# Optimization experiments

Measured on AMD Instinct MI355X. Metric: run time of the kernel, lower is better.

The kernel has to match this reference:

```python
import jax, jax.numpy as jnp
import numpy as np

D_MODEL = 1024
NUM_HEADS = 16
D_K = D_MODEL // NUM_HEADS
B, S = 2, 2048


def setup_inputs() -> dict:
    key = jax.random.key(0)
    ks = jax.random.split(key, 9)
    scale = 1.0 / np.sqrt(D_MODEL)
    return {
        "hidden_states": jax.random.normal(ks[0], (B, S, D_MODEL), dtype=jnp.float32),
        "attention_mask": jnp.ones((B, S, S), dtype=jnp.int32),
        "Wq": jax.random.normal(ks[1], (D_MODEL, D_MODEL), dtype=jnp.float32) * scale,
        "bq": jnp.zeros((D_MODEL,), dtype=jnp.float32),
        "Wk": jax.random.normal(ks[2], (D_MODEL, D_MODEL), dtype=jnp.float32) * scale,
        "bk": jnp.zeros((D_MODEL,), dtype=jnp.float32),
        "Wv": jax.random.normal(ks[3], (D_MODEL, D_MODEL), dtype=jnp.float32) * scale,
        "bv": jnp.zeros((D_MODEL,), dtype=jnp.float32),
        "Wo": jax.random.normal(ks[4], (D_MODEL, D_MODEL), dtype=jnp.float32) * scale,
        "bo": jnp.zeros((D_MODEL,), dtype=jnp.float32),
    }


def reference(hidden_states, attention_mask, Wq, bq, Wk, bk, Wv, bv, Wo, bo):
    b, s, _ = hidden_states.shape
    # torch Linear: y = x @ W.T + b
    def proj(W, bias):
        y = jnp.einsum('bsd,ed->bse', hidden_states, W) + bias
        return y.reshape(b, s, NUM_HEADS, D_K).transpose(0, 2, 1, 3)  # [B,H,S,dk]
    q = proj(Wq, bq)
    k = proj(Wk, bk)
    v = proj(Wv, bv)
    scores = jnp.einsum('bnqd,bnkd->bnqk', q, k) / np.sqrt(D_K)
    mask = attention_mask[:, None, :, :]  # [B,1,S,S]
    scores = jnp.where(mask == 0, jnp.float32(-1e9), scores)
    attn = jax.nn.softmax(scores, axis=-1)  # dropout = identity (eval)
    ctx = jnp.einsum('bnqk,bnkd->bnqd', attn, v)
    ctx = ctx.transpose(0, 2, 1, 3).reshape(b, s, D_MODEL)
    return jnp.einsum('bsd,ed->bse', ctx, Wo) + bo
```

## Files before the change

### kernel.cpp

```cpp
#include <hip/hip_runtime.h>

typedef short short8 __attribute__((ext_vector_type(8)));
typedef float floatx4 __attribute__((ext_vector_type(4)));
typedef float floatx16 __attribute__((ext_vector_type(16)));
typedef unsigned short ushort4v __attribute__((ext_vector_type(4)));

#define DEV static __device__ __forceinline__

DEV unsigned short f2bf(float f) {
  unsigned int u = __builtin_bit_cast(unsigned int, f);
  u += 0x7fffu + ((u >> 16) & 1u);
  return (unsigned short)(u >> 16);
}

DEV unsigned int cvtpk(float a, float b) {
  unsigned int r;
  asm("v_cvt_pk_bf16_f32 %0, %1, %2" : "=v"(r) : "v"(a), "v"(b));
  return r;
}

DEV void gload16(const unsigned short* g, unsigned short* l) {
  __builtin_amdgcn_global_load_lds((__attribute__((address_space(1))) void*)g,
                                   (__attribute__((address_space(3))) void*)l,
                                   16, 0, 0);
}

__global__ void convert_kernel(const float* __restrict__ hs, const float* __restrict__ Wq,
                               const float* __restrict__ Wk, const float* __restrict__ Wv,
                               const float* __restrict__ Wo,
                               unsigned short* __restrict__ xbf, unsigned short* __restrict__ wqkv,
                               unsigned short* __restrict__ wobf) {
  size_t i4 = ((size_t)blockIdx.x * 256 + threadIdx.x) * 4;
  const float* src;
  unsigned short* dst;
  if (i4 < 4194304) {
    src = hs + i4; dst = xbf + i4;
  } else if (i4 < 7340032) {
    size_t o = i4 - 4194304;
    size_t lo = o & 1048575;
    src = (o < 1048576) ? (Wq + lo) : ((o < 2097152) ? (Wk + lo) : (Wv + lo));
    dst = wqkv + o;
  } else {
    size_t o = i4 - 7340032;
    src = Wo + o; dst = wobf + o;
  }
  float4 v = *(const float4*)src;
  ushort4v u;
  u.x = f2bf(v.x); u.y = f2bf(v.y); u.z = f2bf(v.z); u.w = f2bf(v.w);
  *(ushort4v*)dst = u;
}

__global__ void maskpack_kernel(const int* __restrict__ mask, unsigned long long* __restrict__ bits) {
  int w = blockIdx.x * 256 + threadIdx.x;
  const int4* p = (const int4*)(mask + (size_t)w * 64);
  unsigned long long r = 0ull;
#pragma unroll
  for (int j = 0; j < 16; ++j) {
    int4 m = p[j];
    r |= (unsigned long long)(m.x != 0) << (j * 4 + 0);
    r |= (unsigned long long)(m.y != 0) << (j * 4 + 1);
    r |= (unsigned long long)(m.z != 0) << (j * 4 + 2);
    r |= (unsigned long long)(m.w != 0) << (j * 4 + 3);
  }
  bits[w] = r;
}

__global__ void __launch_bounds__(256) qkv_gemm(
    const unsigned short* __restrict__ X, const unsigned short* __restrict__ W,
    const float* __restrict__ bq, const float* __restrict__ bk, const float* __restrict__ bv,
    unsigned short* __restrict__ Qb, unsigned short* __restrict__ Kb,
    unsigned short* __restrict__ Vt) {
  __shared__ __align__(16) unsigned short As[128 * 32];
  __shared__ __align__(16) unsigned short Bs[128 * 32];
  const int tid = threadIdx.x;
  const int lane = tid & 63, wv = tid >> 6;
  const int wm = wv >> 1, wn = wv & 1;
  const int quad = lane >> 4, l15 = lane & 15;
  const int mb = blockIdx.y, nb = blockIdx.x;
  const bool sw = (nb < 16);

  const unsigned short* ga = X + (size_t)(mb * 128 + (tid >> 2)) * 1024 + (tid & 3) * 8;
  const unsigned short* gb = W + (size_t)(nb * 128 + (tid >> 2)) * 1024 + (tid & 3) * 8;
  unsigned short* la1 = As + tid * 8;
  unsigned short* la2 = As + 2048 + tid * 8;
  unsigned short* lb1 = Bs + tid * 8;
  unsigned short* lb2 = Bs + 2048 + tid * 8;

  const int wx = sw ? wn : wm;
  const int ww = sw ? wm : wn;

  floatx4 acc[4][4] = {};
  for (int kt = 0; kt < 32; ++kt) {
    const int k0 = kt * 32;
    gload16(ga + k0, la1);
    gload16(ga + k0 + 65536, la2);
    gload16(gb + k0, lb1);
    gload16(gb + k0 + 65536, lb2);
    __syncthreads();
    short8 xa[4], wb[4];
#pragma unroll
    for (int i = 0; i < 4; ++i) {
      xa[i] = *(const short8*)&As[(wx * 64 + i * 16 + l15) * 32 + quad * 8];
      wb[i] = *(const short8*)&Bs[(ww * 64 + i * 16 + l15) * 32 + quad * 8];
    }
    if (sw) {
#pragma unroll
      for (int mt = 0; mt < 4; ++mt)
#pragma unroll
        for (int nt = 0; nt < 4; ++nt)
          acc[mt][nt] = __builtin_amdgcn_mfma_f32_16x16x32_bf16(wb[mt], xa[nt], acc[mt][nt], 0, 0, 0);
    } else {
#pragma unroll
      for (int mt = 0; mt < 4; ++mt)
#pragma unroll
        for (int nt = 0; nt < 4; ++nt)
          acc[mt][nt] = __builtin_amdgcn_mfma_f32_16x16x32_bf16(xa[mt], wb[nt], acc[mt][nt], 0, 0, 0);
    }
    __syncthreads();
  }

  if (sw) {
#pragma unroll
    for (int mt = 0; mt < 4; ++mt) {
      const int wc0 = nb * 128 + wm * 64 + mt * 16 + quad * 4;
      const int mat = wc0 >> 10;
      const int nl0 = wc0 & 1023;
      const int hh = nl0 >> 6, d0 = nl0 & 63;
      const float4 b4 = *(const float4*)((mat ? bk : bq) + nl0);
      unsigned short* dst = mat ? Kb : Qb;
#pragma unroll
      for (int nt = 0; nt < 4; ++nt) {
        const int colx = mb * 128 + wn * 64 + nt * 16 + l15;
        const int bb = colx >> 11, s = colx & 2047;
        ushort4v pv;
        pv[0] = f2bf(acc[mt][nt][0] + b4.x);
        pv[1] = f2bf(acc[mt][nt][1] + b4.y);
        pv[2] = f2bf(acc[mt][nt][2] + b4.z);
        pv[3] = f2bf(acc[mt][nt][3] + b4.w);
        *(ushort4v*)&dst[((size_t)(bb * 16 + hh) * 2048 + s) * 64 + d0] = pv;
      }
    }
  } else {
#pragma unroll
    for (int nt = 0; nt < 4; ++nt) {
      const int col = nb * 128 + wn * 64 + nt * 16 + l15;
      const int nl = col & 1023;
      const float bias = bv[nl];
      const int hh = nl >> 6, d = nl & 63;
#pragma unroll
      for (int mt = 0; mt < 4; ++mt) {
        const int row0 = mb * 128 + wm * 64 + mt * 16 + quad * 4;
        const int bb = row0 >> 11, s = row0 & 2047;
        ushort4v pv;
#pragma unroll
        for (int r = 0; r < 4; ++r) pv[r] = f2bf(acc[mt][nt][r] + bias);
        *(ushort4v*)&Vt[((size_t)(bb * 16 + hh) * 64 + d) * 2048 + s] = pv;
      }
    }
  }
}

__global__ void __launch_bounds__(256, 2) attn_kernel(
    const unsigned short* __restrict__ Qb, const unsigned short* __restrict__ Kb,
    const unsigned short* __restrict__ Vt, const unsigned long long* __restrict__ mbits,
    unsigned short* __restrict__ ctx) {
  __shared__ __align__(16) unsigned short SM[16384];
  const int tid = threadIdx.x;
  const int lane = tid & 63, wv = tid >> 6;
  const int l31 = lane & 31, h = lane >> 5;
  const int qg = wv & 1, h2 = wv >> 1;
  const int bid = (blockIdx.x & 7) * 128 + (blockIdx.x >> 3);
  const int pair = bid >> 5, qt = bid & 31;
  const int b_ = pair >> 4, hd = pair & 15;
  const int qrow = qt * 64 + qg * 32 + l31;
  const size_t pbase = (size_t)pair * (2048 * 64);
  const size_t vtb = (size_t)pair * (64 * 2048);

  short8 qf[4];
#pragma unroll
  for (int ks = 0; ks < 4; ++ks)
    qf[ks] = *(const short8*)(Qb + pbase + (size_t)qrow * 64 + ks * 16 + h * 8);

  const int kSrc = (lane >> 3) * 64 + (((lane & 7) ^ (lane >> 3)) * 8);
  const int vSrc = (lane >> 2) * 2048 + (((lane & 3) ^ ((lane >> 3) & 3)) * 8);

  const unsigned short* kgb = Kb + pbase + (size_t)h2 * (1024 * 64);
  const unsigned short* vgb = Vt + vtb + h2 * 1024;
  unsigned short* ldK = SM + h2 * 4096 + lane * 8;
  unsigned short* ldV = SM + h2 * 4096 + 2048 + lane * 8;

  const unsigned long long* mrow = mbits + ((size_t)b_ * 2048 + qrow) * 32 + h2 * 16;

  floatx16 acc_o[2] = {};
  float lsum = 0.f;
  const float SCL = 0.125f * 1.44269504088896340736f;
  const float NC = -10.0f;

  if (qg == 0) {
#pragma unroll
    for (int i = 0; i < 4; ++i) gload16(kgb + kSrc + i * 512, ldK + i * 512);
  } else {
#pragma unroll
    for (int i = 0; i < 4; ++i) gload16(vgb + vSrc + (size_t)i * 32768, ldV + i * 512);
  }
  __syncthreads();

  for (int it = 0; it < 32; ++it) {
    const int cur = it & 1;
    const unsigned short* Kh = SM + cur * 8192 + h2 * 4096;
    const unsigned short* Vh = Kh + 2048;

    if (it < 31) {
      const int nb = cur ^ 1;
      if (qg == 0) {
        const unsigned short* s = kgb + (size_t)(it + 1) * 2048 + kSrc;
        unsigned short* d = ldK + nb * 8192;
#pragma unroll
        for (int i = 0; i < 4; ++i) gload16(s + i * 512, d + i * 512);
      } else {
        const unsigned short* s = vgb + (size_t)(it + 1) * 32 + vSrc;
        unsigned short* d = ldV + nb * 8192;
#pragma unroll
        for (int i = 0; i < 4; ++i) gload16(s + (size_t)i * 32768, d + i * 512);
      }
    }
    const unsigned long long w = mrow[it >> 1];
    const int bitbase = (it & 1) * 32;

    floatx16 accs = {};
    __builtin_amdgcn_s_setprio(1);
#pragma unroll
    for (int ks = 0; ks < 4; ++ks) {
      short8 kf = *(const short8*)&Kh[l31 * 64 + (((ks * 2 + h) ^ (l31 & 7)) * 8)];
      accs = __builtin_amdgcn_mfma_f32_32x32x16_bf16(kf, qf[ks], accs, 0, 0, 0);
    }
    __builtin_amdgcn_s_setprio(0);

    if (__any(w != ~0ull)) {
#pragma unroll
      for (int reg = 0; reg < 16; ++reg) {
        const int kl = (reg & 3) + 8 * (reg >> 2) + 4 * h;
        if (!((w >> (bitbase + kl)) & 1ull)) accs[reg] = -6e9f;
      }
    }

    unsigned int pk[8];
    float ls = 0.f;
#pragma unroll
    for (int i = 0; i < 8; ++i) {
      const float a = exp2f(fmaf(accs[2 * i], SCL, NC));
      const float b = exp2f(fmaf(accs[2 * i + 1], SCL, NC));
      ls += a + b;
      pk[i] = cvtpk(a, b);
    }
    lsum += ls;
#pragma unroll
    for (int u = 0; u < 2; ++u) {
      auto r02 = __builtin_amdgcn_permlane32_swap(pk[4 * u + 0], pk[4 * u + 2], false, false);
      auto r13 = __builtin_amdgcn_permlane32_swap(pk[4 * u + 1], pk[4 * u + 3], false, false);
      union { unsigned int wd[4]; short8 s8; } af;
      af.wd[0] = r02[0];
      af.wd[1] = r13[0];
      af.wd[2] = r02[1];
      af.wd[3] = r13[1];
      __builtin_amdgcn_s_setprio(1);
#pragma unroll
      for (int nt = 0; nt < 2; ++nt) {
        const int vrow = nt * 32 + l31;
        short8 vf = *(const short8*)&Vh[vrow * 32 + (((u * 2 + h) ^ ((vrow >> 1) & 3)) * 8)];
        acc_o[nt] = __builtin_amdgcn_mfma_f32_32x32x16_bf16(af.s8, vf, acc_o[nt], 0, 0, 0);
      }
      __builtin_amdgcn_s_setprio(0);
    }
    __syncthreads();
  }

  lsum += __shfl_xor(lsum, 32);

  float* red = (float*)SM;
  if (h2 == 1) {
    float* p = red + (qg * 64 + lane) * 33;
#pragma unroll
    for (int reg = 0; reg < 16; ++reg) {
      p[reg] = acc_o[0][reg];
      p[16 + reg] = acc_o[1][reg];
    }
    p[32] = lsum;
  }
  __syncthreads();
  if (h2 == 0) {
    const float* p = red + (qg * 64 + lane) * 33;
#pragma unroll
    for (int reg = 0; reg < 16; ++reg) {
      acc_o[0][reg] += p[reg];
      acc_o[1][reg] += p[16 + reg];
    }
    lsum += p[32];
    const float rinv = 1.f / ((lsum > 0.f) ? lsum : 1.f);
#pragma unroll
    for (int reg = 0; reg < 16; ++reg) {
      const int ql = (reg & 3) + 8 * (reg >> 2) + 4 * h;
      const float rl = __shfl(rinv, ql);
      const size_t base = ((size_t)b_ * 2048 + qt * 64 + qg * 32 + ql) * 1024 + hd * 64;
      ctx[base + l31]      = f2bf(acc_o[0][reg] * rl);
      ctx[base + 32 + l31] = f2bf(acc_o[1][reg] * rl);
    }
  }
}

__global__ void __launch_bounds__(256) out_gemm(
    const unsigned short* __restrict__ C, const unsigned short* __restrict__ W,
    const float* __restrict__ bo, float* __restrict__ out) {
  __shared__ __align__(16) unsigned short As[128 * 32];
  __shared__ __align__(16) unsigned short Bs[128 * 32];
  const int tid = threadIdx.x;
  const int lane = tid & 63, wv = tid >> 6;
  const int wm = wv >> 1, wn = wv & 1;
  const int quad = lane >> 4, l15 = lane & 15;
  const int mb = blockIdx.y, nb = blockIdx.x;

  const unsigned short* ga = C + (size_t)(mb * 128 + (tid >> 2)) * 1024 + (tid & 3) * 8;
  const unsigned short* gb = W + (size_t)(nb * 128 + (tid >> 2)) * 1024 + (tid & 3) * 8;
  unsigned short* la1 = As + tid * 8;
  unsigned short* la2 = As + 2048 + tid * 8;
  unsigned short* lb1 = Bs + tid * 8;
  unsigned short* lb2 = Bs + 2048 + tid * 8;

  floatx4 acc[4][4] = {};
  for (int kt = 0; kt < 32; ++kt) {
    const int k0 = kt * 32;
    gload16(ga + k0, la1);
    gload16(ga + k0 + 65536, la2);
    gload16(gb + k0, lb1);
    gload16(gb + k0 + 65536, lb2);
    __syncthreads();
    short8 af[4], bfr[4];
#pragma unroll
    for (int i = 0; i < 4; ++i) {
      af[i]  = *(const short8*)&As[(wm * 64 + i * 16 + l15) * 32 + quad * 8];
      bfr[i] = *(const short8*)&Bs[(wn * 64 + i * 16 + l15) * 32 + quad * 8];
    }
#pragma unroll
    for (int mt = 0; mt < 4; ++mt)
#pragma unroll
      for (int nt = 0; nt < 4; ++nt)
        acc[mt][nt] = __builtin_amdgcn_mfma_f32_16x16x32_bf16(af[mt], bfr[nt], acc[mt][nt], 0, 0, 0);
    __syncthreads();
  }
#pragma unroll
  for (int nt = 0; nt < 4; ++nt) {
    const int col = nb * 128 + wn * 64 + nt * 16 + l15;
    const float bias = bo[col];
#pragma unroll
    for (int mt = 0; mt < 4; ++mt)
#pragma unroll
      for (int r = 0; r < 4; ++r) {
        const int row = mb * 128 + wm * 64 + mt * 16 + quad * 4 + r;
        out[(size_t)row * 1024 + col] = acc[mt][nt][r] + bias;
      }
  }
}

extern "C" void kernel_launch(void* const* d_in, const int* in_sizes, int n_in,
                              void* d_out, int out_size, void* d_ws, size_t ws_size,
                              hipStream_t stream) {
  const float* hs = (const float*)d_in[0];
  const int* mask = (const int*)d_in[1];
  const float* Wq = (const float*)d_in[2];
  const float* bq = (const float*)d_in[3];
  const float* Wk = (const float*)d_in[4];
  const float* bk = (const float*)d_in[5];
  const float* Wv = (const float*)d_in[6];
  const float* bv = (const float*)d_in[7];
  const float* Wo = (const float*)d_in[8];
  const float* bo = (const float*)d_in[9];
  float* out = (float*)d_out;

  char* ws = (char*)d_ws;
  unsigned short* xbf  = (unsigned short*)(ws + 0);
  unsigned short* wqkv = (unsigned short*)(ws + 8388608);
  unsigned short* wobf = (unsigned short*)(ws + 14680064);
  unsigned short* Qb   = (unsigned short*)(ws + 16777216);
  unsigned short* Kb   = (unsigned short*)(ws + 25165824);
  unsigned short* Vt   = (unsigned short*)(ws + 33554432);
  unsigned short* ctx  = (unsigned short*)(ws + 41943040);
  unsigned long long* mbits = (unsigned long long*)(ws + 50331648);

  convert_kernel<<<8192, 256, 0, stream>>>(hs, Wq, Wk, Wv, Wo, xbf, wqkv, wobf);
  maskpack_kernel<<<512, 256, 0, stream>>>(mask, mbits);
  qkv_gemm<<<dim3(24, 32), 256, 0, stream>>>(xbf, wqkv, bq, bk, bv, Qb, Kb, Vt);
  attn_kernel<<<1024, 256, 0, stream>>>(Qb, Kb, Vt, mbits, ctx);
  out_gemm<<<dim3(8, 32), 256, 0, stream>>>(ctx, wobf, bo, out);
}
```

Before: 254.9 us.

## Store K/V in MFMA-fragment order and load them directly into registers

The projection epilogue now writes K and V^T in a pre-tiled layout that matches the MFMA operand fragments, so each lane can fetch its fragments with contiguous 16-byte global loads. The attention kernel drops the LDS double-buffer, the async global-to-LDS copies and the per-iteration barrier, and instead software-prefetches the next tile's fragments into registers. The risk is that the two wave pairs sharing a query block now each read K/V from global/L2 with no LDS sharing. It also raises register pressure and exposes global-load latency more directly.

```diff
diff --git a/kernel.cpp b/kernel.cpp
--- a/kernel.cpp
+++ b/kernel.cpp
@@ -127,7 +127,6 @@
       const int nl0 = wc0 & 1023;
       const int hh = nl0 >> 6, d0 = nl0 & 63;
       const float4 b4 = *(const float4*)((mat ? bk : bq) + nl0);
-      unsigned short* dst = mat ? Kb : Qb;
 #pragma unroll
       for (int nt = 0; nt < 4; ++nt) {
         const int colx = mb * 128 + wn * 64 + nt * 16 + l15;
@@ -137,7 +136,13 @@
         pv[1] = f2bf(acc[mt][nt][1] + b4.y);
         pv[2] = f2bf(acc[mt][nt][2] + b4.z);
         pv[3] = f2bf(acc[mt][nt][3] + b4.w);
-        *(ushort4v*)&dst[((size_t)(bb * 16 + hh) * 2048 + s) * 64 + d0] = pv;
+        if (mat == 0) {
+          *(ushort4v*)&Qb[((size_t)(bb * 16 + hh) * 2048 + s) * 64 + d0] = pv;
+        } else {
+          const size_t idx = (size_t)(bb * 16 + hh) * 131072 + (s >> 5) * 2048 +
+                             (d0 >> 4) * 512 + (((d0 >> 3) & 1) * 32 + (s & 31)) * 8 + (d0 & 7);
+          *(ushort4v*)&Kb[idx] = pv;
+        }
       }
     }
   } else {
@@ -150,11 +155,14 @@
 #pragma unroll
       for (int mt = 0; mt < 4; ++mt) {
         const int row0 = mb * 128 + wm * 64 + mt * 16 + quad * 4;
-        const int bb = row0 >> 11, s = row0 & 2047;
+        const int bb = row0 >> 11, s0 = row0 & 2047;
         ushort4v pv;
 #pragma unroll
         for (int r = 0; r < 4; ++r) pv[r] = f2bf(acc[mt][nt][r] + bias);
-        *(ushort4v*)&Vt[((size_t)(bb * 16 + hh) * 64 + d) * 2048 + s] = pv;
+        const size_t idx = (size_t)(bb * 16 + hh) * 131072 + (s0 >> 5) * 2048 +
+                           ((s0 >> 4) & 1) * 1024 + (d >> 5) * 512 +
+                           (((s0 >> 3) & 1) * 32 + (d & 31)) * 8 + (s0 & 7);
+        *(ushort4v*)&Vt[idx] = pv;
       }
     }
   }
@@ -164,7 +172,7 @@
     const unsigned short* __restrict__ Qb, const unsigned short* __restrict__ Kb,
     const unsigned short* __restrict__ Vt, const unsigned long long* __restrict__ mbits,
     unsigned short* __restrict__ ctx) {
-  __shared__ __align__(16) unsigned short SM[16384];
+  __shared__ float red[2 * 64 * 33];
   const int tid = threadIdx.x;
   const int lane = tid & 63, wv = tid >> 6;
   const int l31 = lane & 31, h = lane >> 5;
@@ -173,68 +181,43 @@
   const int pair = bid >> 5, qt = bid & 31;
   const int b_ = pair >> 4, hd = pair & 15;
   const int qrow = qt * 64 + qg * 32 + l31;
-  const size_t pbase = (size_t)pair * (2048 * 64);
-  const size_t vtb = (size_t)pair * (64 * 2048);
 
   short8 qf[4];
 #pragma unroll
   for (int ks = 0; ks < 4; ++ks)
-    qf[ks] = *(const short8*)(Qb + pbase + (size_t)qrow * 64 + ks * 16 + h * 8);
-
-  const int kSrc = (lane >> 3) * 64 + (((lane & 7) ^ (lane >> 3)) * 8);
-  const int vSrc = (lane >> 2) * 2048 + (((lane & 3) ^ ((lane >> 3) & 3)) * 8);
-
-  const unsigned short* kgb = Kb + pbase + (size_t)h2 * (1024 * 64);
-  const unsigned short* vgb = Vt + vtb + h2 * 1024;
-  unsigned short* ldK = SM + h2 * 4096 + lane * 8;
-  unsigned short* ldV = SM + h2 * 4096 + 2048 + lane * 8;
+    qf[ks] = *(const short8*)(Qb + (size_t)pair * 131072 + (size_t)qrow * 64 + ks * 16 + h * 8);
+
+  const unsigned short* kp = Kb + (size_t)pair * 131072 + h2 * 65536 + lane * 8;
+  const unsigned short* vp = Vt + (size_t)pair * 131072 + h2 * 65536 + lane * 8;
 
   const unsigned long long* mrow = mbits + ((size_t)b_ * 2048 + qrow) * 32 + h2 * 16;
+
+  short8 kf[4], vf[4];
+#pragma unroll
+  for (int i = 0; i < 4; ++i) kf[i] = *(const short8*)(kp + i * 512);
+#pragma unroll
+  for (int i = 0; i < 4; ++i) vf[i] = *(const short8*)(vp + i * 512);
 
   floatx16 acc_o[2] = {};
   float lsum = 0.f;
   const float SCL = 0.125f * 1.44269504088896340736f;
   const float NC = -10.0f;
 
-  if (qg == 0) {
-#pragma unroll
-    for (int i = 0; i < 4; ++i) gload16(kgb + kSrc + i * 512, ldK + i * 512);
-  } else {
-#pragma unroll
-    for (int i = 0; i < 4; ++i) gload16(vgb + vSrc + (size_t)i * 32768, ldV + i * 512);
-  }
-  __syncthreads();
-
+#pragma unroll 2
   for (int it = 0; it < 32; ++it) {
-    const int cur = it & 1;
-    const unsigned short* Kh = SM + cur * 8192 + h2 * 4096;
-    const unsigned short* Vh = Kh + 2048;
-
-    if (it < 31) {
-      const int nb = cur ^ 1;
-      if (qg == 0) {
-        const unsigned short* s = kgb + (size_t)(it + 1) * 2048 + kSrc;
-        unsigned short* d = ldK + nb * 8192;
-#pragma unroll
-        for (int i = 0; i < 4; ++i) gload16(s + i * 512, d + i * 512);
-      } else {
-        const unsigned short* s = vgb + (size_t)(it + 1) * 32 + vSrc;
-        unsigned short* d = ldV + nb * 8192;
-#pragma unroll
-        for (int i = 0; i < 4; ++i) gload16(s + (size_t)i * 32768, d + i * 512);
-      }
-    }
     const unsigned long long w = mrow[it >> 1];
     const int bitbase = (it & 1) * 32;
 
     floatx16 accs = {};
     __builtin_amdgcn_s_setprio(1);
 #pragma unroll
-    for (int ks = 0; ks < 4; ++ks) {
-      short8 kf = *(const short8*)&Kh[l31 * 64 + (((ks * 2 + h) ^ (l31 & 7)) * 8)];
-      accs = __builtin_amdgcn_mfma_f32_32x32x16_bf16(kf, qf[ks], accs, 0, 0, 0);
-    }
+    for (int ks = 0; ks < 4; ++ks)
+      accs = __builtin_amdgcn_mfma_f32_32x32x16_bf16(kf[ks], qf[ks], accs, 0, 0, 0);
     __builtin_amdgcn_s_setprio(0);
+
+    kp += 2048;
+#pragma unroll
+    for (int i = 0; i < 4; ++i) kf[i] = *(const short8*)(kp + i * 512);
 
     if (__any(w != ~0ull)) {
 #pragma unroll
@@ -265,19 +248,18 @@
       af.wd[3] = r13[1];
       __builtin_amdgcn_s_setprio(1);
 #pragma unroll
-      for (int nt = 0; nt < 2; ++nt) {
-        const int vrow = nt * 32 + l31;
-        short8 vf = *(const short8*)&Vh[vrow * 32 + (((u * 2 + h) ^ ((vrow >> 1) & 3)) * 8)];
-        acc_o[nt] = __builtin_amdgcn_mfma_f32_32x32x16_bf16(af.s8, vf, acc_o[nt], 0, 0, 0);
-      }
+      for (int nt = 0; nt < 2; ++nt)
+        acc_o[nt] = __builtin_amdgcn_mfma_f32_32x32x16_bf16(af.s8, vf[u * 2 + nt], acc_o[nt], 0, 0, 0);
       __builtin_amdgcn_s_setprio(0);
     }
-    __syncthreads();
+
+    vp += 2048;
+#pragma unroll
+    for (int i = 0; i < 4; ++i) vf[i] = *(const short8*)(vp + i * 512);
   }
 
   lsum += __shfl_xor(lsum, 32);
 
-  float* red = (float*)SM;
   if (h2 == 1) {
     float* p = red + (qg * 64 + lane) * 33;
 #pragma unroll
```

Result: faster. 247.8 us (-2.8%).
